# Kernel optimization log

Measured on AMD Instinct MI355X. Metric: run time of the kernel, lower is better.

## Reference

```python
import jax, jax.numpy as jnp
import numpy as np

N = 100000
E = 1600000
F = 128
H = 4
D = 32  # emb_dim // heads
C = 2
NEG_SLOPE = 0.2


def setup_inputs() -> dict:
    key = jax.random.key(0)
    ks = jax.random.split(key, 16)
    inp = {
        "x": jax.random.normal(ks[0], (N, F), dtype=jnp.float32),
        "src": jax.random.randint(ks[1], (E,), 0, N, dtype=jnp.int32),
        "dst": jax.random.randint(ks[2], (E,), 0, N, dtype=jnp.int32),
        # layer 1 params (in=F, out=H*D)
        "W1": jax.random.normal(ks[3], (F, H * D), dtype=jnp.float32) * 0.05,
        "al1": jax.random.normal(ks[4], (H, D), dtype=jnp.float32) * 0.05,
        "ar1": jax.random.normal(ks[5], (H, D), dtype=jnp.float32) * 0.05,
        "b1": jnp.zeros((H * D,), dtype=jnp.float32),
        # layer 2 params (in=H*D, out=H*D)
        "W2": jax.random.normal(ks[6], (H * D, H * D), dtype=jnp.float32) * 0.05,
        "al2": jax.random.normal(ks[7], (H, D), dtype=jnp.float32) * 0.05,
        "ar2": jax.random.normal(ks[8], (H, D), dtype=jnp.float32) * 0.05,
        "b2": jnp.zeros((H * D,), dtype=jnp.float32),
        # final classifier
        "Wf": jax.random.normal(ks[9], (H * D, C), dtype=jnp.float32) * 0.05,
        "bf": jnp.zeros((C,), dtype=jnp.float32),
    }
    return inp


def gat_layer(x, src, dst, W, attn_l, attn_r, bias):
    # Linear projection, split into heads: [N, H, D]
    h = (x @ W).reshape(N, H, D)
    # Per-node attention terms: [N, H]
    el = jnp.einsum("nhd,hd->nh", h, attn_l)
    er = jnp.einsum("nhd,hd->nh", h, attn_r)
    # Per-edge logits with LeakyReLU(0.2): [E, H]
    e = jax.nn.leaky_relu(el[src] + er[dst], negative_slope=NEG_SLOPE)
    # Numerically stable edge-softmax over incoming edges of each dst node
    m = jax.ops.segment_max(e, dst, num_segments=N)
    m = jnp.where(jnp.isfinite(m), m, 0.0)  # nodes with no in-edges
    a = jnp.exp(e - m[dst])
    denom = jax.ops.segment_sum(a, dst, num_segments=N)
    alpha = a / jnp.maximum(denom[dst], 1e-9)
    # Weighted message aggregation: scatter-add over dst -> [N, H, D]
    out = jax.ops.segment_sum(h[src] * alpha[:, :, None], dst, num_segments=N)
    out = out + bias.reshape(H, D)
    # is_concat=True: reshape heads into feature dim -> [N, H*D]
    return out.reshape(N, H * D)


def reference(x, src, dst, W1, al1, ar1, b1, W2, al2, ar2, b2, Wf, bf):
    h = gat_layer(x, src, dst, W1, al1, ar1, b1)
    h = gat_layer(h, src, dst, W2, al2, ar2, b2)
    # prediction=True: final linear layer (note: self.activation is never used in forward)
    return h @ Wf + bf
```

## Files before the change

kernel.cpp:

```cpp
#include <hip/hip_runtime.h>
#include <hip/hip_fp16.h>

#define NN 100000
#define EE 1600000
#define NPB 256
#define EPB (EE / NPB)
#define NGRP2 200
#define GR2 (NN / NGRP2)
#define CCAP 10240
#define PSB 50

typedef _Float16 f16x8 __attribute__((ext_vector_type(8)));
typedef float f32x4 __attribute__((ext_vector_type(4)));

__global__ __launch_bounds__(256) void wtrans_k(const float* __restrict__ W1,
                                                const float* __restrict__ W2,
                                                __half* __restrict__ Wt1,
                                                __half* __restrict__ Wt2) {
    int b = blockIdx.x;
    const float* W = (b & 1) ? W2 : W1;
    __half* Wt = (b & 1) ? Wt2 : Wt1;
    int t = (b >> 1) * 256 + threadIdx.x;
    int k = t >> 7, n = t & 127;
    Wt[n * 128 + k] = __float2half(W[k * 128 + n]);
}

template <int INHALF>
__global__ __launch_bounds__(256) void gemm_el_k(const void* __restrict__ Xv,
                                                 const __half* __restrict__ Wt,
                                                 const float* __restrict__ al,
                                                 const float* __restrict__ ar,
                                                 __half* __restrict__ Hout,
                                                 float* __restrict__ el,
                                                 float* __restrict__ er) {
    __shared__ alignas(16) unsigned short Xs[64 * 128];
    __shared__ alignas(16) unsigned short Ws[128 * 128];
    int t = threadIdx.x;
    int row0 = blockIdx.x * 64;

    {
        const uint4* g = (const uint4*)Wt;
#pragma unroll
        for (int j = 0; j < 8; ++j) {
            int c = j * 256 + t;
            uint4 v = g[c];
            int n = c >> 4, kb = (c & 15) << 4;
            *(uint4*)((char*)Ws + n * 256 + (kb ^ ((n & 7) << 4))) = v;
        }
    }
#pragma unroll
    for (int j = 0; j < 4; ++j) {
        int c = j * 256 + t;
        int row = c >> 4, kb = (c & 15) << 4;
        int grow = row0 + row; if (grow >= NN) grow = NN - 1;
        uint4 pk;
        if (INHALF) {
            pk = ((const uint4*)Xv)[(size_t)grow * 16 + (c & 15)];
        } else {
            const float4* xp = (const float4*)Xv + (size_t)grow * 32 + (c & 15) * 2;
            float4 v0 = xp[0], v1 = xp[1];
            __half2 h01 = __floats2half2_rn(v0.x, v0.y);
            __half2 h23 = __floats2half2_rn(v0.z, v0.w);
            __half2 h45 = __floats2half2_rn(v1.x, v1.y);
            __half2 h67 = __floats2half2_rn(v1.z, v1.w);
            pk = make_uint4(__builtin_bit_cast(unsigned, h01),
                            __builtin_bit_cast(unsigned, h23),
                            __builtin_bit_cast(unsigned, h45),
                            __builtin_bit_cast(unsigned, h67));
        }
        *(uint4*)((char*)Xs + row * 256 + (kb ^ ((row & 7) << 4))) = pk;
    }
    __syncthreads();

    int w = t >> 6, lane = t & 63;
    int lr = lane & 15, lg = lane >> 4;
    int xrow = w * 16 + lr;

    f32x4 acc[8] = {};
#pragma unroll
    for (int ks = 0; ks < 4; ++ks) {
        int kb = ks * 64 + lg * 16;
        f16x8 b = *(const f16x8*)((char*)Xs + xrow * 256 + (kb ^ ((xrow & 7) << 4)));
#pragma unroll
        for (int ct = 0; ct < 8; ++ct) {
            int wrow = ct * 16 + lr;
            f16x8 a = *(const f16x8*)((char*)Ws + wrow * 256 + (kb ^ ((wrow & 7) << 4)));
            acc[ct] = __builtin_amdgcn_mfma_f32_16x16x32_f16(a, b, acc[ct], 0, 0, 0);
        }
    }

    int grow = row0 + w * 16 + lr;
    bool valid = grow < NN;
    if (valid) {
        __half* hp = Hout + (size_t)grow * 128 + lg * 4;
#pragma unroll
        for (int ct = 0; ct < 8; ++ct) {
            __half2 p0 = __floats2half2_rn(acc[ct][0], acc[ct][1]);
            __half2 p1 = __floats2half2_rn(acc[ct][2], acc[ct][3]);
            uint2 pk = make_uint2(__builtin_bit_cast(unsigned, p0),
                                  __builtin_bit_cast(unsigned, p1));
            *(uint2*)(hp + ct * 16) = pk;
        }
    }
    float pl[4] = {}, pr[4] = {};
#pragma unroll
    for (int ct = 0; ct < 8; ++ct) {
        int hd = ct >> 1;
        float4 a_l = *(const float4*)&al[ct * 16 + lg * 4];
        float4 a_r = *(const float4*)&ar[ct * 16 + lg * 4];
        pl[hd] += acc[ct][0] * a_l.x + acc[ct][1] * a_l.y +
                  acc[ct][2] * a_l.z + acc[ct][3] * a_l.w;
        pr[hd] += acc[ct][0] * a_r.x + acc[ct][1] * a_r.y +
                  acc[ct][2] * a_r.z + acc[ct][3] * a_r.w;
    }
#pragma unroll
    for (int hd = 0; hd < 4; ++hd) {
        pl[hd] += __shfl_xor(pl[hd], 16, 64);
        pl[hd] += __shfl_xor(pl[hd], 32, 64);
        pr[hd] += __shfl_xor(pr[hd], 16, 64);
        pr[hd] += __shfl_xor(pr[hd], 32, 64);
    }
    if (lg == 0 && valid) {
        *(float4*)&el[grow * 4] = make_float4(pl[0], pl[1], pl[2], pl[3]);
        *(float4*)&er[grow * 4] = make_float4(pr[0], pr[1], pr[2], pr[3]);
    }
}

__global__ __launch_bounds__(512) void partA_k(const int* __restrict__ dst,
                                               int* __restrict__ gcnt) {
    __shared__ int cnt[NGRP2];
    int b = blockIdx.x, t = threadIdx.x;
    for (int i = t; i < NGRP2; i += 512) cnt[i] = 0;
    __syncthreads();
    int e_beg = b * EPB;
    for (int e = e_beg + t; e < e_beg + EPB; e += 512)
        atomicAdd(&cnt[dst[e] / GR2], 1);
    __syncthreads();
    for (int i = t; i < NGRP2; i += 512) gcnt[i * NPB + b] = cnt[i];
}

__global__ __launch_bounds__(1024) void psumA_k(const int* __restrict__ gcnt,
                                                int* __restrict__ psum) {
    __shared__ int sh[1024];
    int b = blockIdx.x, t = threadIdx.x;
    sh[t] = gcnt[b * 1024 + t];
    __syncthreads();
    for (int off = 512; off; off >>= 1) {
        if (t < off) sh[t] += sh[t + off];
        __syncthreads();
    }
    if (t == 0) psum[b] = sh[0];
}

__global__ __launch_bounds__(64) void psumB_k(const int* __restrict__ psum,
                                              int* __restrict__ poffb,
                                              int* __restrict__ rowptr) {
    __shared__ int sh[64];
    int t = threadIdx.x;
    int v = (t < PSB) ? psum[t] : 0;
    sh[t] = v;
    __syncthreads();
    for (int off = 1; off < 64; off <<= 1) {
        int u = (t >= off) ? sh[t - off] : 0;
        __syncthreads();
        sh[t] += u;
        __syncthreads();
    }
    if (t < PSB) poffb[t] = sh[t] - v;
    if (t == 0) rowptr[NN] = EE;
}

__global__ __launch_bounds__(1024) void psumC_k(const int* __restrict__ gcnt,
                                                const int* __restrict__ poffb,
                                                int* __restrict__ poff) {
    __shared__ int sh[1024];
    int b = blockIdx.x, t = threadIdx.x;
    int v = gcnt[b * 1024 + t];
    sh[t] = v;
    __syncthreads();
    for (int off = 1; off < 1024; off <<= 1) {
        int u = (t >= off) ? sh[t - off] : 0;
        __syncthreads();
        sh[t] += u;
        __syncthreads();
    }
    poff[b * 1024 + t] = sh[t] - v + poffb[b];
}

__global__ __launch_bounds__(512) void partB_k(const int* __restrict__ src,
                                               const int* __restrict__ dst,
                                               const int* __restrict__ poff,
                                               int* __restrict__ ebuf) {
    __shared__ int cur[NGRP2];
    int b = blockIdx.x, t = threadIdx.x;
    for (int i = t; i < NGRP2; i += 512) cur[i] = poff[i * NPB + b];
    __syncthreads();
    int e_beg = b * EPB;
    for (int e = e_beg + t; e < e_beg + EPB; e += 512) {
        int d = dst[e], s = src[e];
        int g = d / GR2;
        int p = atomicAdd(&cur[g], 1);
        ebuf[p] = s | ((d - g * GR2) << 17);
    }
}

__global__ __launch_bounds__(512) void partC_k(const int* __restrict__ ebuf,
                                               const int* __restrict__ poff,
                                               int* __restrict__ rowptr,
                                               int* __restrict__ csr_src) {
    __shared__ int lsrc[CCAP];
    __shared__ int ldeg[512];
    __shared__ int ssc[512];
    __shared__ int lcur[512];
    int g = blockIdx.x, t = threadIdx.x;
    int nbase = g * GR2;
    int beg = poff[g * NPB];
    int end = (g == NGRP2 - 1) ? EE : poff[(g + 1) * NPB];
    ldeg[t] = 0;
    __syncthreads();
    for (int e = beg + t; e < end; e += 512)
        atomicAdd(&ldeg[ebuf[e] >> 17], 1);
    __syncthreads();
    int v = ldeg[t];
    ssc[t] = v;
    __syncthreads();
    for (int off = 1; off < 512; off <<= 1) {
        int u = (t >= off) ? ssc[t - off] : 0;
        __syncthreads();
        ssc[t] += u;
        __syncthreads();
    }
    int ex = ssc[t] - v;
    lcur[t] = ex;
    if (t < GR2) rowptr[nbase + t] = beg + ex;
    __syncthreads();
    for (int e = beg + t; e < end; e += 512) {
        int pk = ebuf[e];
        int p = atomicAdd(&lcur[pk >> 17], 1);
        if (p < CCAP) lsrc[p] = pk & 0x1FFFF;
    }
    __syncthreads();
    int len = end - beg; if (len > CCAP) len = CCAP;
    for (int i = t; i < len; i += 512) csr_src[beg + i] = lsrc[i];
}

#define BC16(x, I) __uint_as_float(__builtin_amdgcn_ds_swizzle( \
    __float_as_uint(x), ((I) << 5) | 0x10))

#define AGG_STEP(av, hvp, I)                      \
    {                                             \
        float ai = BC16(av, I);                   \
        float2 f = __half22float2((hvp)[I]);      \
        acc0 = fmaf(ai, f.x, acc0);               \
        acc1 = fmaf(ai, f.y, acc1);               \
    }

#define AGG16(av, hvp)                                                       \
    AGG_STEP(av, hvp, 0)  AGG_STEP(av, hvp, 1)  AGG_STEP(av, hvp, 2)         \
    AGG_STEP(av, hvp, 3)  AGG_STEP(av, hvp, 4)  AGG_STEP(av, hvp, 5)         \
    AGG_STEP(av, hvp, 6)  AGG_STEP(av, hvp, 7)  AGG_STEP(av, hvp, 8)         \
    AGG_STEP(av, hvp, 9)  AGG_STEP(av, hvp, 10) AGG_STEP(av, hvp, 11)        \
    AGG_STEP(av, hvp, 12) AGG_STEP(av, hvp, 13) AGG_STEP(av, hvp, 14)        \
    AGG_STEP(av, hvp, 15)

template <int FINAL>
__global__ __launch_bounds__(64) void gat_agg_k(const int* __restrict__ rowptr,
                                                const int* __restrict__ csr_src,
                                                const float* __restrict__ el,
                                                const float* __restrict__ er,
                                                const __half* __restrict__ h,
                                                const float* __restrict__ bias,
                                                void* __restrict__ outv,
                                                const float* __restrict__ Wf,
                                                const float* __restrict__ bf) {
    int wave = blockIdx.x;
    int lane = threadIdx.x;
    int row = rowptr[wave], end = rowptr[wave + 1];
    int hd = lane >> 4, sub = lane & 15;
    float erd = er[wave * 4 + hd];
    const __half2* hbase = (const __half2*)h + lane;

    float dpart = 0.f, acc0 = 0.f, acc1 = 0.f;
    for (int base = row; base < end; base += 32) {
        int c = end - base;
        int s0 = csr_src[base + (sub < c ? sub : 0)];
        float a0 = 0.f;
        {
            float v = el[s0 * 4 + hd] + erd;
            v = (v >= 0.f) ? v : 0.2f * v;
            if (sub < c) a0 = __expf(v);
        }
        if (c > 16) {
            int i1 = 16 + sub;
            int s1 = csr_src[base + (i1 < c ? i1 : 0)];
            float a1 = 0.f;
            {
                float v = el[s1 * 4 + hd] + erd;
                v = (v >= 0.f) ? v : 0.2f * v;
                if (i1 < c) a1 = __expf(v);
            }
            dpart += a0 + a1;
            __half2 hv[32];
#pragma unroll
            for (int i = 0; i < 16; ++i) {
                int si = __builtin_amdgcn_readlane(s0, i);
                hv[i] = hbase[si * 64];
            }
#pragma unroll
            for (int i = 0; i < 16; ++i) {
                int si = __builtin_amdgcn_readlane(s1, i);
                hv[16 + i] = hbase[si * 64];
            }
            AGG16(a0, hv)
            AGG16(a1, (hv + 16))
        } else {
            dpart += a0;
            __half2 hv[16];
#pragma unroll
            for (int i = 0; i < 16; ++i) {
                int si = __builtin_amdgcn_readlane(s0, i);
                hv[i] = hbase[si * 64];
            }
            AGG16(a0, hv)
        }
    }
    float denom = dpart;
#pragma unroll
    for (int off = 1; off < 16; off <<= 1) denom += __shfl_xor(denom, off, 64);
    float inv = 1.f / fmaxf(denom, 1e-9f);
    float2 bv = *(const float2*)&bias[lane * 2];
    float o0 = acc0 * inv + bv.x;
    float o1 = acc1 * inv + bv.y;

    if (FINAL) {
        float* out = (float*)outv;
        float4 wf = *(const float4*)&Wf[lane * 4];
        float c0 = o0 * wf.x + o1 * wf.z;
        float c1 = o0 * wf.y + o1 * wf.w;
#pragma unroll
        for (int off = 1; off < 64; off <<= 1) {
            c0 += __shfl_xor(c0, off, 64);
            c1 += __shfl_xor(c1, off, 64);
        }
        if (lane == 0) {
            float2 res = make_float2(c0 + bf[0], c1 + bf[1]);
            *(float2*)&out[(size_t)wave * 2] = res;
        }
    } else {
        __half* out = (__half*)outv;
        *(__half2*)&out[(size_t)wave * 128 + lane * 2] = __floats2half2_rn(o0, o1);
    }
}

extern "C" void kernel_launch(void* const* d_in, const int* in_sizes, int n_in,
                              void* d_out, int out_size, void* d_ws, size_t ws_size,
                              hipStream_t stream) {
    const float* x   = (const float*)d_in[0];
    const int*   src = (const int*)d_in[1];
    const int*   dst = (const int*)d_in[2];
    const float* W1  = (const float*)d_in[3];
    const float* al1 = (const float*)d_in[4];
    const float* ar1 = (const float*)d_in[5];
    const float* b1  = (const float*)d_in[6];
    const float* W2  = (const float*)d_in[7];
    const float* al2 = (const float*)d_in[8];
    const float* ar2 = (const float*)d_in[9];
    const float* b2  = (const float*)d_in[10];
    const float* Wf  = (const float*)d_in[11];
    const float* bf  = (const float*)d_in[12];
    float* out = (float*)d_out;

    __half* bufH  = (__half*)d_ws;
    __half* bufO  = bufH + (size_t)NN * 128;
    float* el     = (float*)(bufO + (size_t)NN * 128);
    float* er     = el + NN * 4;
    int* rowptr   = (int*)(er + NN * 4);
    int* csr_src  = rowptr + NN + 2;
    int* ebuf     = csr_src + EE;
    int* gcnt     = ebuf + EE;
    int* poff     = gcnt + NGRP2 * NPB;
    int* psum     = poff + NGRP2 * NPB;
    int* poffb    = psum + PSB;
    __half* Wt1   = (__half*)(poffb + PSB);
    __half* Wt2   = Wt1 + 128 * 128;

    const int T = 256;
    int gGemm = (NN + 63) / 64;

    wtrans_k<<<128, T, 0, stream>>>(W1, W2, Wt1, Wt2);
    partA_k<<<NPB, 512, 0, stream>>>(dst, gcnt);
    psumA_k<<<PSB, 1024, 0, stream>>>(gcnt, psum);
    psumB_k<<<1, 64, 0, stream>>>(psum, poffb, rowptr);
    psumC_k<<<PSB, 1024, 0, stream>>>(gcnt, poffb, poff);
    partB_k<<<NPB, 512, 0, stream>>>(src, dst, poff, ebuf);
    partC_k<<<NGRP2, 512, 0, stream>>>(ebuf, poff, rowptr, csr_src);

    gemm_el_k<0><<<gGemm, T, 0, stream>>>(x, Wt1, al1, ar1, bufH, el, er);
    gat_agg_k<0><<<NN, 64, 0, stream>>>(rowptr, csr_src, el, er, bufH, b1, bufO,
                                        nullptr, nullptr);
    gemm_el_k<1><<<gGemm, T, 0, stream>>>(bufO, Wt2, al2, ar2, bufH, el, er);
    gat_agg_k<1><<<NN, 64, 0, stream>>>(rowptr, csr_src, el, er, bufH, b2, out,
                                        Wf, bf);
}
```

Baseline: 221.2 us.

## Double GEMM row tile per block and fold weight transpose into partition kernel

The projection GEMM now handles 128 rows per block, with each wave computing two 16-row tiles. Each weight fragment read from LDS feeds two MFMAs, and the 32KB W tile is loaded half as many times across the grid. The separate weight-transpose kernel is removed; its work runs in 16 extra blocks appended to the edge-count partition kernel, saving one launch. The trade-offs are higher LDS use (64KB per block), which lowers occupancy, more accumulator registers, and fewer GEMM blocks.

Measured after the change: 221.3 us. About the same (+0.0%).

```diff
diff --git a/kernel.cpp b/kernel.cpp
--- a/kernel.cpp
+++ b/kernel.cpp
@@ -13,18 +13,6 @@
 typedef _Float16 f16x8 __attribute__((ext_vector_type(8)));
 typedef float f32x4 __attribute__((ext_vector_type(4)));
 
-__global__ __launch_bounds__(256) void wtrans_k(const float* __restrict__ W1,
-                                                const float* __restrict__ W2,
-                                                __half* __restrict__ Wt1,
-                                                __half* __restrict__ Wt2) {
-    int b = blockIdx.x;
-    const float* W = (b & 1) ? W2 : W1;
-    __half* Wt = (b & 1) ? Wt2 : Wt1;
-    int t = (b >> 1) * 256 + threadIdx.x;
-    int k = t >> 7, n = t & 127;
-    Wt[n * 128 + k] = __float2half(W[k * 128 + n]);
-}
-
 template <int INHALF>
 __global__ __launch_bounds__(256) void gemm_el_k(const void* __restrict__ Xv,
                                                  const __half* __restrict__ Wt,
@@ -33,10 +21,10 @@
                                                  __half* __restrict__ Hout,
                                                  float* __restrict__ el,
                                                  float* __restrict__ er) {
-    __shared__ alignas(16) unsigned short Xs[64 * 128];
+    __shared__ alignas(16) unsigned short Xs[128 * 128];
     __shared__ alignas(16) unsigned short Ws[128 * 128];
     int t = threadIdx.x;
-    int row0 = blockIdx.x * 64;
+    int row0 = blockIdx.x * 128;
 
     {
         const uint4* g = (const uint4*)Wt;
@@ -49,7 +37,7 @@
         }
     }
 #pragma unroll
-    for (int j = 0; j < 4; ++j) {
+    for (int j = 0; j < 8; ++j) {
         int c = j * 256 + t;
         int row = c >> 4, kb = (c & 15) << 4;
         int grow = row0 + row; if (grow >= NN) grow = NN - 1;
@@ -74,60 +62,83 @@
 
     int w = t >> 6, lane = t & 63;
     int lr = lane & 15, lg = lane >> 4;
-    int xrow = w * 16 + lr;
-
-    f32x4 acc[8] = {};
+
+    f32x4 acc[2][8] = {};
 #pragma unroll
     for (int ks = 0; ks < 4; ++ks) {
         int kb = ks * 64 + lg * 16;
-        f16x8 b = *(const f16x8*)((char*)Xs + xrow * 256 + (kb ^ ((xrow & 7) << 4)));
+        int xr0 = w * 32 + lr, xr1 = w * 32 + 16 + lr;
+        f16x8 b0 = *(const f16x8*)((char*)Xs + xr0 * 256 + (kb ^ ((xr0 & 7) << 4)));
+        f16x8 b1 = *(const f16x8*)((char*)Xs + xr1 * 256 + (kb ^ ((xr1 & 7) << 4)));
 #pragma unroll
         for (int ct = 0; ct < 8; ++ct) {
             int wrow = ct * 16 + lr;
             f16x8 a = *(const f16x8*)((char*)Ws + wrow * 256 + (kb ^ ((wrow & 7) << 4)));
-            acc[ct] = __builtin_amdgcn_mfma_f32_16x16x32_f16(a, b, acc[ct], 0, 0, 0);
-        }
-    }
-
-    int grow = row0 + w * 16 + lr;
-    bool valid = grow < NN;
-    if (valid) {
-        __half* hp = Hout + (size_t)grow * 128 + lg * 4;
+            acc[0][ct] = __builtin_amdgcn_mfma_f32_16x16x32_f16(a, b0, acc[0][ct], 0, 0, 0);
+            acc[1][ct] = __builtin_amdgcn_mfma_f32_16x16x32_f16(a, b1, acc[1][ct], 0, 0, 0);
+        }
+    }
+
+#pragma unroll
+    for (int rt = 0; rt < 2; ++rt) {
+        int grow = row0 + w * 32 + rt * 16 + lr;
+        bool valid = grow < NN;
+        if (valid) {
+            __half* hp = Hout + (size_t)grow * 128 + lg * 4;
+#pragma unroll
+            for (int ct = 0; ct < 8; ++ct) {
+                __half2 p0 = __floats2half2_rn(acc[rt][ct][0], acc[rt][ct][1]);
+                __half2 p1 = __floats2half2_rn(acc[rt][ct][2], acc[rt][ct][3]);
+                uint2 pk = make_uint2(__builtin_bit_cast(unsigned, p0),
+                                      __builtin_bit_cast(unsigned, p1));
+                *(uint2*)(hp + ct * 16) = pk;
+            }
+        }
+        float pl[4] = {}, pr[4] = {};
 #pragma unroll
         for (int ct = 0; ct < 8; ++ct) {
-            __half2 p0 = __floats2half2_rn(acc[ct][0], acc[ct][1]);
-            __half2 p1 = __floats2half2_rn(acc[ct][2], acc[ct][3]);
-            uint2 pk = make_uint2(__builtin_bit_cast(unsigned, p0),
-                                  __builtin_bit_cast(unsigned, p1));
-            *(uint2*)(hp + ct * 16) = pk;
-        }
-    }
-    float pl[4] = {}, pr[4] = {};
-#pragma unroll
-    for (int ct = 0; ct < 8; ++ct) {
-        int hd = ct >> 1;
-        float4 a_l = *(const float4*)&al[ct * 16 + lg * 4];
-        float4 a_r = *(const float4*)&ar[ct * 16 + lg * 4];
-        pl[hd] += acc[ct][0] * a_l.x + acc[ct][1] * a_l.y +
-                  acc[ct][2] * a_l.z + acc[ct][3] * a_l.w;
-        pr[hd] += acc[ct][0] * a_r.x + acc[ct][1] * a_r.y +
-                  acc[ct][2] * a_r.z + acc[ct][3] * a_r.w;
-    }
-#pragma unroll
-    for (int hd = 0; hd < 4; ++hd) {
-        pl[hd] += __shfl_xor(pl[hd], 16, 64);
-        pl[hd] += __shfl_xor(pl[hd], 32, 64);
-        pr[hd] += __shfl_xor(pr[hd], 16, 64);
-        pr[hd] += __shfl_xor(pr[hd], 32, 64);
-    }
-    if (lg == 0 && valid) {
-        *(float4*)&el[grow * 4] = make_float4(pl[0], pl[1], pl[2], pl[3]);
-        *(float4*)&er[grow * 4] = make_float4(pr[0], pr[1], pr[2], pr[3]);
+            int hd = ct >> 1;
+            float4 a_l = *(const float4*)&al[ct * 16 + lg * 4];
+            float4 a_r = *(const float4*)&ar[ct * 16 + lg * 4];
+            pl[hd] += acc[rt][ct][0] * a_l.x + acc[rt][ct][1] * a_l.y +
+                      acc[rt][ct][2] * a_l.z + acc[rt][ct][3] * a_l.w;
+            pr[hd] += acc[rt][ct][0] * a_r.x + acc[rt][ct][1] * a_r.y +
+                      acc[rt][ct][2] * a_r.z + acc[rt][ct][3] * a_r.w;
+        }
+#pragma unroll
+        for (int hd = 0; hd < 4; ++hd) {
+            pl[hd] += __shfl_xor(pl[hd], 16, 64);
+            pl[hd] += __shfl_xor(pl[hd], 32, 64);
+            pr[hd] += __shfl_xor(pr[hd], 16, 64);
+            pr[hd] += __shfl_xor(pr[hd], 32, 64);
+        }
+        if (lg == 0 && valid) {
+            *(float4*)&el[grow * 4] = make_float4(pl[0], pl[1], pl[2], pl[3]);
+            *(float4*)&er[grow * 4] = make_float4(pr[0], pr[1], pr[2], pr[3]);
+        }
     }
 }
 
 __global__ __launch_bounds__(512) void partA_k(const int* __restrict__ dst,
-                                               int* __restrict__ gcnt) {
+                                               int* __restrict__ gcnt,
+                                               const float* __restrict__ W1,
+                                               const float* __restrict__ W2,
+                                               __half* __restrict__ Wt1,
+                                               __half* __restrict__ Wt2) {
+    if (blockIdx.x >= NPB) {
+        int b = blockIdx.x - NPB;
+#pragma unroll
+        for (int i = 0; i < 4; ++i) {
+            int t4 = b * 2048 + i * 512 + threadIdx.x;
+            int layer = t4 >> 14;
+            int idx = t4 & 16383;
+            int k = idx >> 7, n = idx & 127;
+            const float* W = layer ? W2 : W1;
+            __half* Wt = layer ? Wt2 : Wt1;
+            Wt[n * 128 + k] = __float2half(W[idx]);
+        }
+        return;
+    }
     __shared__ int cnt[NGRP2];
     int b = blockIdx.x, t = threadIdx.x;
     for (int i = t; i < NGRP2; i += 512) cnt[i] = 0;
@@ -385,10 +396,9 @@
     __half* Wt2   = Wt1 + 128 * 128;
 
     const int T = 256;
-    int gGemm = (NN + 63) / 64;
-
-    wtrans_k<<<128, T, 0, stream>>>(W1, W2, Wt1, Wt2);
-    partA_k<<<NPB, 512, 0, stream>>>(dst, gcnt);
+    int gGemm = (NN + 127) / 128;
+
+    partA_k<<<NPB + 16, 512, 0, stream>>>(dst, gcnt, W1, W2, Wt1, Wt2);
     psumA_k<<<PSB, 1024, 0, stream>>>(gcnt, psum);
     psumB_k<<<1, 64, 0, stream>>>(psum, poffb, rowptr);
     psumC_k<<<PSB, 1024, 0, stream>>>(gcnt, poffb, poff);
```
